# Performance work log

Hardware: AMD Instinct MI355X
Metric: run time of the kernel (lower is better)

The kernel has to match this reference:

```python
import jax, jax.numpy as jnp
import numpy as np

N_NODES = 50000
N_EDGES = 800000
IN_FEATS = 96
HIDDEN = 48


def setup_inputs() -> dict:
    key = jax.random.key(0)
    ks = jax.random.split(key, 16)
    x = jax.random.normal(ks[0], (N_NODES, IN_FEATS), dtype=jnp.float32)
    edge_index = jax.random.randint(ks[1], (2, N_EDGES), 0, N_NODES, dtype=jnp.int32)

    def lin(k, fan_in, fan_out):
        s = 1.0 / np.sqrt(fan_in)
        return jax.random.uniform(k, (fan_in, fan_out), jnp.float32, -s, s)

    return {
        "x": x,
        "edge_index": edge_index,
        # SAGEConv layer 0: in -> hidden
        "w_self0": lin(ks[2], IN_FEATS, HIDDEN),
        "w_neigh0": lin(ks[3], IN_FEATS, HIDDEN),
        "b0": jnp.zeros((HIDDEN,), jnp.float32),
        # SAGEConv layer 1: hidden -> hidden
        "w_self1": lin(ks[4], HIDDEN, HIDDEN),
        "w_neigh1": lin(ks[5], HIDDEN, HIDDEN),
        "b1": jnp.zeros((HIDDEN,), jnp.float32),
        # SAGEConv layer 2: hidden -> hidden
        "w_self2": lin(ks[6], HIDDEN, HIDDEN),
        "w_neigh2": lin(ks[7], HIDDEN, HIDDEN),
        "b2": jnp.zeros((HIDDEN,), jnp.float32),
        # prediction head: hidden -> 1
        "w_pred": lin(ks[8], HIDDEN, 1),
        "b_pred": jnp.zeros((1,), jnp.float32),
    }


def _sage_mean(x, src, dst, deg_inv, w_self, w_neigh, b):
    # mean over in-neighbors: gather src features, segment-sum at dst, / in-degree
    agg = jax.ops.segment_sum(x[src], dst, num_segments=N_NODES) * deg_inv  # [N, F]
    return x @ w_self + agg @ w_neigh + b


def reference(x, edge_index, w_self0, w_neigh0, b0, w_self1, w_neigh1, b1,
              w_self2, w_neigh2, b2, w_pred, b_pred):
    src, dst = edge_index[0], edge_index[1]
    deg = jax.ops.segment_sum(jnp.ones((src.shape[0],), x.dtype), dst,
                              num_segments=N_NODES)
    deg_inv = (1.0 / jnp.maximum(deg, 1.0))[:, None]  # isolated nodes -> 0 agg

    h = jax.nn.relu(_sage_mean(x, src, dst, deg_inv, w_self0, w_neigh0, b0))
    h = jax.nn.relu(_sage_mean(h, src, dst, deg_inv, w_self1, w_neigh1, b1))
    h = jax.nn.relu(_sage_mean(h, src, dst, deg_inv, w_self2, w_neigh2, b2))
    return h @ w_pred + b_pred  # [N, 1]
```

## Files before the change

kernel.cpp:

```cpp
#include <hip/hip_runtime.h>
#include <hip/hip_fp16.h>


constexpr int HID = 48;
constexpr int MAXDEG = 64;
constexpr int RSTRIDE = 64;
constexpr int GNB = 64;

__device__ __forceinline__ unsigned pack_h2(float a, float b) {
    __half2 h = __floats2half2_rn(a, b);
    return *reinterpret_cast<unsigned*>(&h);
}
__device__ __forceinline__ void acc_u2(float* g, uint2 u) {
    __half2 h0 = *reinterpret_cast<__half2*>(&u.x);
    __half2 h1 = *reinterpret_cast<__half2*>(&u.y);
    float2 f0 = __half22float2(h0), f1 = __half22float2(h1);
    g[0] += f0.x; g[1] += f0.y; g[2] += f1.x; g[3] += f1.y;
}
__device__ __forceinline__ void unpack_u2(float* v, uint2 u) {
    __half2 h0 = *reinterpret_cast<__half2*>(&u.x);
    __half2 h1 = *reinterpret_cast<__half2*>(&u.y);
    float2 f0 = __half22float2(h0), f1 = __half22float2(h1);
    v[0] = f0.x; v[1] = f0.y; v[2] = f1.x; v[3] = f1.y;
}
__device__ __forceinline__ void fma12_h(const uint2* __restrict__ wrow, float s,
                                        float* acc) {
    uint2 w0 = wrow[0], w1 = wrow[1], w2 = wrow[2];
    float v[12];
    unpack_u2(v + 0, w0); unpack_u2(v + 4, w1); unpack_u2(v + 8, w2);
#pragma unroll
    for (int j = 0; j < 12; ++j) acc[j] = fmaf(s, v[j], acc[j]);
}

template <int NB>
__device__ __forceinline__ void gather_pad(const __half* __restrict__ p,
                                           const unsigned short* __restrict__ bkt,
                                           const uint4 (&pw)[NB], int deg, int e,
                                           int jb, int zrow, float* g) {
    float ga[12], gb[12];
#pragma unroll
    for (int j = 0; j < 12; ++j) { ga[j] = 0.0f; gb[j] = 0.0f; }
    const int sh = 16 * e;
#pragma unroll
    for (int b = 0; b < NB; ++b) {
        const int k0 = 8 * b + e;
        int i0 = (k0 < deg)     ? (int)((pw[b].x >> sh) & 0xffffu) : zrow;
        int i1 = (k0 + 2 < deg) ? (int)((pw[b].y >> sh) & 0xffffu) : zrow;
        int i2 = (k0 + 4 < deg) ? (int)((pw[b].z >> sh) & 0xffffu) : zrow;
        int i3 = (k0 + 6 < deg) ? (int)((pw[b].w >> sh) & 0xffffu) : zrow;
        const uint2* r0 = reinterpret_cast<const uint2*>(p + (size_t)i0 * RSTRIDE + jb);
        const uint2* r1 = reinterpret_cast<const uint2*>(p + (size_t)i1 * RSTRIDE + jb);
        const uint2* r2 = reinterpret_cast<const uint2*>(p + (size_t)i2 * RSTRIDE + jb);
        const uint2* r3 = reinterpret_cast<const uint2*>(p + (size_t)i3 * RSTRIDE + jb);
        uint2 a0 = r0[0], a1 = r0[1], a2 = r0[2];
        uint2 b0 = r1[0], b1 = r1[1], b2 = r1[2];
        uint2 c0 = r2[0], c1 = r2[1], c2 = r2[2];
        uint2 d0 = r3[0], d1 = r3[1], d2 = r3[2];
        acc_u2(ga + 0, a0); acc_u2(ga + 4, a1); acc_u2(ga + 8, a2);
        acc_u2(gb + 0, b0); acc_u2(gb + 4, b1); acc_u2(gb + 8, b2);
        acc_u2(ga + 0, c0); acc_u2(ga + 4, c1); acc_u2(ga + 8, c2);
        acc_u2(gb + 0, d0); acc_u2(gb + 4, d1); acc_u2(gb + 8, d2);
    }
    int i = 8 * NB + e;
    for (; i + 6 < deg; i += 8) {
        int s0 = bkt[i], s1 = bkt[i + 2], s2 = bkt[i + 4], s3 = bkt[i + 6];
        const uint2* r0 = reinterpret_cast<const uint2*>(p + (size_t)s0 * RSTRIDE + jb);
        const uint2* r1 = reinterpret_cast<const uint2*>(p + (size_t)s1 * RSTRIDE + jb);
        const uint2* r2 = reinterpret_cast<const uint2*>(p + (size_t)s2 * RSTRIDE + jb);
        const uint2* r3 = reinterpret_cast<const uint2*>(p + (size_t)s3 * RSTRIDE + jb);
        uint2 a0 = r0[0], a1 = r0[1], a2 = r0[2];
        uint2 b0 = r1[0], b1 = r1[1], b2 = r1[2];
        uint2 c0 = r2[0], c1 = r2[1], c2 = r2[2];
        uint2 d0 = r3[0], d1 = r3[1], d2 = r3[2];
        acc_u2(ga + 0, a0); acc_u2(ga + 4, a1); acc_u2(ga + 8, a2);
        acc_u2(gb + 0, b0); acc_u2(gb + 4, b1); acc_u2(gb + 8, b2);
        acc_u2(ga + 0, c0); acc_u2(ga + 4, c1); acc_u2(ga + 8, c2);
        acc_u2(gb + 0, d0); acc_u2(gb + 4, d1); acc_u2(gb + 8, d2);
    }
    for (; i + 2 < deg; i += 4) {
        int s0 = bkt[i], s1 = bkt[i + 2];
        const uint2* r0 = reinterpret_cast<const uint2*>(p + (size_t)s0 * RSTRIDE + jb);
        const uint2* r1 = reinterpret_cast<const uint2*>(p + (size_t)s1 * RSTRIDE + jb);
        uint2 a0 = r0[0], a1 = r0[1], a2 = r0[2];
        uint2 b0 = r1[0], b1 = r1[1], b2 = r1[2];
        acc_u2(ga + 0, a0); acc_u2(ga + 4, a1); acc_u2(ga + 8, a2);
        acc_u2(gb + 0, b0); acc_u2(gb + 4, b1); acc_u2(gb + 8, b2);
    }
    if (i < deg) {
        const uint2* r0 = reinterpret_cast<const uint2*>(p + (size_t)bkt[i] * RSTRIDE + jb);
        uint2 a0 = r0[0], a1 = r0[1], a2 = r0[2];
        acc_u2(ga + 0, a0); acc_u2(ga + 4, a1); acc_u2(ga + 8, a2);
    }
#pragma unroll
    for (int j = 0; j < 12; ++j) g[j] = ga[j] + gb[j];
#pragma unroll
    for (int j = 0; j < 12; ++j) g[j] += __shfl_xor(g[j], 4, 64);
}

__global__ __launch_bounds__(128) void fill_proj_k(
    const float* __restrict__ X, const float* __restrict__ Wn,
    __half* __restrict__ p_out, int n_nodes,
    const int* __restrict__ src, const int* __restrict__ dst,
    int* __restrict__ cnt, unsigned short* __restrict__ buckets,
    int n_edges, int gemm_blocks, int cstride) {
    __shared__ float wlds[96 * HID];
    const int t = threadIdx.x;

    if ((int)blockIdx.x >= gemm_blocks) {
        int base = (blockIdx.x - gemm_blocks) * 512 + t;
#pragma unroll
        for (int u = 0; u < 4; ++u) {
            int eidx = base + u * 128;
            if (eidx < n_edges) {
                int d = dst[eidx];
                int s = src[eidx];
                int pos = atomicAdd(&cnt[(size_t)d * cstride], 1);
                if (pos < MAXDEG) buckets[(size_t)d * MAXDEG + pos] = (unsigned short)s;
            }
        }
        return;
    }

    if (blockIdx.x == 0 && t < 32)
        reinterpret_cast<unsigned*>(p_out + (size_t)n_nodes * RSTRIDE)[t] = 0u;

    const int q = t & 3;
    const int m = t >> 2;
    const int jb = q * 12;
    const int n0 = blockIdx.x * GNB + 2 * m;
    const int n1 = n0 + 1;
    const bool v0 = n0 < n_nodes, v1 = n1 < n_nodes;
    const int cn0 = v0 ? n0 : 0, cn1 = v1 ? n1 : 0;
    const float4* xr0 = reinterpret_cast<const float4*>(X + (size_t)cn0 * 96);
    const float4* xr1 = reinterpret_cast<const float4*>(X + (size_t)cn1 * 96);

    for (int i = t; i < 96 * HID; i += 128) wlds[i] = Wn[i];
    __syncthreads();

    float pa[12], pb[12];
#pragma unroll
    for (int j = 0; j < 12; ++j) { pa[j] = 0.0f; pb[j] = 0.0f; }
#pragma unroll 4
    for (int k4 = 0; k4 < 24; ++k4) {
        float4 xa = xr0[k4];
        float4 xb = xr1[k4];
#pragma unroll
        for (int c = 0; c < 4; ++c) {
            float x0 = (c == 0) ? xa.x : (c == 1) ? xa.y : (c == 2) ? xa.z : xa.w;
            float x1 = (c == 0) ? xb.x : (c == 1) ? xb.y : (c == 2) ? xb.z : xb.w;
            const float4* wr =
                reinterpret_cast<const float4*>(&wlds[(k4 * 4 + c) * HID + jb]);
#pragma unroll
            for (int j4 = 0; j4 < 3; ++j4) {
                float4 wv = wr[j4];
                pa[j4 * 4 + 0] = fmaf(x0, wv.x, pa[j4 * 4 + 0]);
                pa[j4 * 4 + 1] = fmaf(x0, wv.y, pa[j4 * 4 + 1]);
                pa[j4 * 4 + 2] = fmaf(x0, wv.z, pa[j4 * 4 + 2]);
                pa[j4 * 4 + 3] = fmaf(x0, wv.w, pa[j4 * 4 + 3]);
                pb[j4 * 4 + 0] = fmaf(x1, wv.x, pb[j4 * 4 + 0]);
                pb[j4 * 4 + 1] = fmaf(x1, wv.y, pb[j4 * 4 + 1]);
                pb[j4 * 4 + 2] = fmaf(x1, wv.z, pb[j4 * 4 + 2]);
                pb[j4 * 4 + 3] = fmaf(x1, wv.w, pb[j4 * 4 + 3]);
            }
        }
    }
    if (v0) {
        uint2* po = reinterpret_cast<uint2*>(p_out + (size_t)n0 * RSTRIDE + jb);
        po[0] = make_uint2(pack_h2(pa[0], pa[1]), pack_h2(pa[2], pa[3]));
        po[1] = make_uint2(pack_h2(pa[4], pa[5]), pack_h2(pa[6], pa[7]));
        po[2] = make_uint2(pack_h2(pa[8], pa[9]), pack_h2(pa[10], pa[11]));
    }
    if (v1) {
        uint2* po = reinterpret_cast<uint2*>(p_out + (size_t)n1 * RSTRIDE + jb);
        po[0] = make_uint2(pack_h2(pb[0], pb[1]), pack_h2(pb[2], pb[3]));
        po[1] = make_uint2(pack_h2(pb[4], pb[5]), pack_h2(pb[6], pb[7]));
        po[2] = make_uint2(pack_h2(pb[8], pb[9]), pack_h2(pb[10], pb[11]));
    }
}

__global__ __launch_bounds__(128, 4) void act_k(
    const __half* __restrict__ p_in, const float* __restrict__ X,
    const float* __restrict__ ws, const float* __restrict__ bias,
    const int* __restrict__ cnt, const unsigned short* __restrict__ buckets,
    __half* __restrict__ h_out, int n_nodes, int cstride) {
    __shared__ float wlds[96 * HID];
    __shared__ float b_lds[HID];

    const int t = threadIdx.x;
    if (blockIdx.x == 0 && t < 32)
        reinterpret_cast<unsigned*>(h_out + (size_t)n_nodes * RSTRIDE)[t] = 0u;

    const int q = t & 3;
    const int e = (t >> 2) & 1;
    const int m = t >> 3;
    const int n = blockIdx.x * 16 + m;
    const bool nv = n < n_nodes;
    const int cn = nv ? n : 0;
    const int jb = q * 12;

    const int deg_raw = cnt[(size_t)cn * cstride];
    const unsigned short* bkt = buckets + (size_t)cn * MAXDEG;
    uint4 pw[4];
#pragma unroll
    for (int b = 0; b < 4; ++b) pw[b] = reinterpret_cast<const uint4*>(bkt)[b];

    for (int i4 = t; i4 < 96 * HID / 4; i4 += 128)
        reinterpret_cast<float4*>(wlds)[i4] = reinterpret_cast<const float4*>(ws)[i4];
    if (t < HID) b_lds[t] = bias[t];
    __syncthreads();

    if (!nv) return;

    const int deg = min(deg_raw, MAXDEG);
    const float di = 1.0f / fmaxf((float)deg, 1.0f);

    float g[12];
    gather_pad<4>(p_in, bkt, pw, deg, e, jb, n_nodes, g);

    float s[12];
#pragma unroll
    for (int j = 0; j < 12; ++j) s[j] = (e == 0) ? b_lds[jb + j] : 0.0f;
    const float4* xr = reinterpret_cast<const float4*>(X + (size_t)cn * 96 + 48 * e);
#pragma unroll 4
    for (int k4 = 0; k4 < 12; ++k4) {
        float4 xv = xr[k4];
#pragma unroll
        for (int c = 0; c < 4; ++c) {
            float xc = (c == 0) ? xv.x : (c == 1) ? xv.y : (c == 2) ? xv.z : xv.w;
            const float4* wr = reinterpret_cast<const float4*>(
                &wlds[(48 * e + k4 * 4 + c) * HID + jb]);
#pragma unroll
            for (int j4 = 0; j4 < 3; ++j4) {
                float4 wv = wr[j4];
                s[j4 * 4 + 0] = fmaf(xc, wv.x, s[j4 * 4 + 0]);
                s[j4 * 4 + 1] = fmaf(xc, wv.y, s[j4 * 4 + 1]);
                s[j4 * 4 + 2] = fmaf(xc, wv.z, s[j4 * 4 + 2]);
                s[j4 * 4 + 3] = fmaf(xc, wv.w, s[j4 * 4 + 3]);
            }
        }
    }
#pragma unroll
    for (int j = 0; j < 12; ++j) s[j] += __shfl_xor(s[j], 4, 64);

    if (e == 0) {
        float h[12];
#pragma unroll
        for (int j = 0; j < 12; ++j) h[j] = fmaxf(fmaf(di, g[j], s[j]), 0.0f);
        uint2* ho = reinterpret_cast<uint2*>(h_out + (size_t)n * RSTRIDE + jb);
        ho[0] = make_uint2(pack_h2(h[0], h[1]), pack_h2(h[2], h[3]));
        ho[1] = make_uint2(pack_h2(h[4], h[5]), pack_h2(h[6], h[7]));
        ho[2] = make_uint2(pack_h2(h[8], h[9]), pack_h2(h[10], h[11]));
    }
}

template <bool LAST>
__global__ __launch_bounds__(128, 6) void layer_k(
    const __half* __restrict__ h_in, const int* __restrict__ cnt,
    const unsigned short* __restrict__ buckets, const float* __restrict__ wn,
    const float* __restrict__ ws, const float* __restrict__ bn,
    const float* __restrict__ w_pred, const float* __restrict__ b_pred,
    __half* __restrict__ h_out, float* __restrict__ out, int n_nodes,
    int cstride) {
    __shared__ uint2 wn_s[HID * HID / 4];
    __shared__ uint2 ws_s[HID * HID / 4];
    __shared__ float bn_lds[HID];
    __shared__ float wp_lds[HID];

    const int t = threadIdx.x;
    const int q = t & 3;
    const int e = (t >> 2) & 1;
    const int m = t >> 3;
    const int n = blockIdx.x * 16 + m;
    const bool nv = n < n_nodes;
    const int cn = nv ? n : 0;
    const int jb = q * 12;

    if (!LAST && blockIdx.x == 0 && t < 32)
        reinterpret_cast<unsigned*>(h_out + (size_t)n_nodes * RSTRIDE)[t] = 0u;

    const int deg_raw = cnt[(size_t)cn * cstride];
    const unsigned short* bkt = buckets + (size_t)cn * MAXDEG;
    uint4 pw[2];
#pragma unroll
    for (int b = 0; b < 2; ++b) pw[b] = reinterpret_cast<const uint4*>(bkt)[b];
    const uint2* hr = reinterpret_cast<const uint2*>(h_in + (size_t)cn * RSTRIDE + jb);
    uint2 ha = hr[0], hb = hr[1], hc = hr[2];

    for (int i4 = t; i4 < HID * HID / 4; i4 += 128) {
        float4 a = reinterpret_cast<const float4*>(wn)[i4];
        float4 b = reinterpret_cast<const float4*>(ws)[i4];
        wn_s[i4] = make_uint2(pack_h2(a.x, a.y), pack_h2(a.z, a.w));
        ws_s[i4] = make_uint2(pack_h2(b.x, b.y), pack_h2(b.z, b.w));
    }
    if (t < HID) bn_lds[t] = bn[t];
    if (LAST && t < HID) wp_lds[t] = w_pred[t];
    __syncthreads();

    if (!nv) return;

    const int deg = min(deg_raw, MAXDEG);
    const float di = 1.0f / fmaxf((float)deg, 1.0f);
    float g[12];
    gather_pad<2>(h_in, bkt, pw, deg, e, jb, n_nodes, g);
#pragma unroll
    for (int j = 0; j < 12; ++j) g[j] *= di;

    float hs_own[12];
    unpack_u2(hs_own + 0, ha); unpack_u2(hs_own + 4, hb); unpack_u2(hs_own + 8, hc);

    float acc[12];
#pragma unroll
    for (int j = 0; j < 12; ++j) acc[j] = (e == 0) ? bn_lds[jb + j] : 0.0f;

    const int kb = e * 24;
#pragma unroll
    for (int kk = 0; kk < 24; ++kk) {
        const int k = kb + kk;
        const int srcl = (t & ~3) | (k / 12);
        float gs = __shfl(g[kk % 12], srcl, 64);
        float hv = __shfl(hs_own[kk % 12], srcl, 64);
        fma12_h(&wn_s[(k * HID + jb) >> 2], gs, acc);
        fma12_h(&ws_s[(k * HID + jb) >> 2], hv, acc);
    }
#pragma unroll
    for (int j = 0; j < 12; ++j) acc[j] += __shfl_xor(acc[j], 4, 64);

    if (LAST) {
        float s = 0.0f;
#pragma unroll
        for (int j = 0; j < 12; ++j) s = fmaf(fmaxf(acc[j], 0.0f), wp_lds[jb + j], s);
        s += __shfl_xor(s, 1, 64);
        s += __shfl_xor(s, 2, 64);
        if ((t & 7) == 0) out[n] = s + b_pred[0];
        return;
    }

    if (e == 0) {
        float h[12];
#pragma unroll
        for (int j = 0; j < 12; ++j) h[j] = fmaxf(acc[j], 0.0f);
        uint2* ho = reinterpret_cast<uint2*>(h_out + (size_t)n * RSTRIDE + jb);
        ho[0] = make_uint2(pack_h2(h[0], h[1]), pack_h2(h[2], h[3]));
        ho[1] = make_uint2(pack_h2(h[4], h[5]), pack_h2(h[6], h[7]));
        ho[2] = make_uint2(pack_h2(h[8], h[9]), pack_h2(h[10], h[11]));
    }
}

extern "C" void kernel_launch(void* const* d_in, const int* in_sizes, int n_in,
                              void* d_out, int out_size, void* d_ws, size_t ws_size,
                              hipStream_t stream) {
    const float* x        = (const float*)d_in[0];
    const int*   ei       = (const int*)d_in[1];
    const float* w_self0  = (const float*)d_in[2];
    const float* w_neigh0 = (const float*)d_in[3];
    const float* b0       = (const float*)d_in[4];
    const float* w_self1  = (const float*)d_in[5];
    const float* w_neigh1 = (const float*)d_in[6];
    const float* b1       = (const float*)d_in[7];
    const float* w_self2  = (const float*)d_in[8];
    const float* w_neigh2 = (const float*)d_in[9];
    const float* b2       = (const float*)d_in[10];
    const float* w_pred   = (const float*)d_in[11];
    const float* b_pred   = (const float*)d_in[12];

    const int n_nodes = in_sizes[0] / 96;
    const int n_edges = in_sizes[1] / 2;
    const int* src = ei;
    const int* dst = ei + n_edges;

    const size_t need_fixed = (size_t)n_nodes * MAXDEG * 2
                            + 3 * ((size_t)(n_nodes + 1) * RSTRIDE * 2);
    int cstride = (need_fixed + (size_t)n_nodes * 4 * 4 <= ws_size) ? 4 : 1;

    char* wsb = (char*)d_ws;
    int* cnt                = (int*)wsb;              wsb += (size_t)n_nodes * cstride * 4;
    unsigned short* buckets = (unsigned short*)wsb;   wsb += (size_t)n_nodes * MAXDEG * 2;
    __half* p0 = (__half*)wsb;                        wsb += (size_t)(n_nodes + 1) * RSTRIDE * 2;
    __half* h1 = (__half*)wsb;                        wsb += (size_t)(n_nodes + 1) * RSTRIDE * 2;
    __half* h2 = (__half*)wsb;                        wsb += (size_t)(n_nodes + 1) * RSTRIDE * 2;
    float* out = (float*)d_out;

    const int gnb = (n_nodes + GNB - 1) / GNB;
    const int fb = (n_edges + 511) / 512;
    const int lb = (n_nodes + 15) / 16;

    hipMemsetAsync(cnt, 0, (size_t)n_nodes * cstride * 4, stream);

    fill_proj_k<<<gnb + fb, 128, 0, stream>>>(x, w_neigh0, p0, n_nodes, src, dst,
                                              cnt, buckets, n_edges, gnb, cstride);
    act_k<<<lb, 128, 0, stream>>>(p0, x, w_self0, b0, cnt, buckets, h1,
                                  n_nodes, cstride);
    layer_k<false><<<lb, 128, 0, stream>>>(h1, cnt, buckets, w_neigh1, w_self1,
                                           b1, nullptr, nullptr, h2, nullptr,
                                           n_nodes, cstride);
    layer_k<true><<<lb, 128, 0, stream>>>(h2, cnt, buckets, w_neigh2, w_self2,
                                          b2, w_pred, b_pred, nullptr, out,
                                          n_nodes, cstride);
}
```

Before: 215.4 us.

## Remap threads to 8-channel slices with 16-byte gathers instead of edge-split halves

Each node's 8 lanes now own 8 output channels each (6 active, 2 idle), and each lane gathers whole 16-byte chunks of every neighbor row. Previously lanes split the edges between two halves, used 8-byte loads and reduced across lanes with shuffles. The goal is wider memory transactions and no cross-lane reduction of the gathered sums. In exchange, 25% of lanes sit idle and each active lane walks every edge serially, so per-lane memory latency chains are longer. The dense projections are reorganized to match, and the layer-0 self projection no longer splits K across two lanes.

```diff
diff --git a/kernel.cpp b/kernel.cpp
--- a/kernel.cpp
+++ b/kernel.cpp
@@ -17,84 +17,66 @@
     float2 f0 = __half22float2(h0), f1 = __half22float2(h1);
     g[0] += f0.x; g[1] += f0.y; g[2] += f1.x; g[3] += f1.y;
 }
+__device__ __forceinline__ void acc_u4(float* g, uint4 u) {
+    acc_u2(g + 0, make_uint2(u.x, u.y));
+    acc_u2(g + 4, make_uint2(u.z, u.w));
+}
 __device__ __forceinline__ void unpack_u2(float* v, uint2 u) {
     __half2 h0 = *reinterpret_cast<__half2*>(&u.x);
     __half2 h1 = *reinterpret_cast<__half2*>(&u.y);
     float2 f0 = __half22float2(h0), f1 = __half22float2(h1);
     v[0] = f0.x; v[1] = f0.y; v[2] = f1.x; v[3] = f1.y;
 }
-__device__ __forceinline__ void fma12_h(const uint2* __restrict__ wrow, float s,
-                                        float* acc) {
-    uint2 w0 = wrow[0], w1 = wrow[1], w2 = wrow[2];
-    float v[12];
-    unpack_u2(v + 0, w0); unpack_u2(v + 4, w1); unpack_u2(v + 8, w2);
-#pragma unroll
-    for (int j = 0; j < 12; ++j) acc[j] = fmaf(s, v[j], acc[j]);
-}
-
-template <int NB>
-__device__ __forceinline__ void gather_pad(const __half* __restrict__ p,
-                                           const unsigned short* __restrict__ bkt,
-                                           const uint4 (&pw)[NB], int deg, int e,
-                                           int jb, int zrow, float* g) {
-    float ga[12], gb[12];
-#pragma unroll
-    for (int j = 0; j < 12; ++j) { ga[j] = 0.0f; gb[j] = 0.0f; }
-    const int sh = 16 * e;
-#pragma unroll
-    for (int b = 0; b < NB; ++b) {
-        const int k0 = 8 * b + e;
-        int i0 = (k0 < deg)     ? (int)((pw[b].x >> sh) & 0xffffu) : zrow;
-        int i1 = (k0 + 2 < deg) ? (int)((pw[b].y >> sh) & 0xffffu) : zrow;
-        int i2 = (k0 + 4 < deg) ? (int)((pw[b].z >> sh) & 0xffffu) : zrow;
-        int i3 = (k0 + 6 < deg) ? (int)((pw[b].w >> sh) & 0xffffu) : zrow;
-        const uint2* r0 = reinterpret_cast<const uint2*>(p + (size_t)i0 * RSTRIDE + jb);
-        const uint2* r1 = reinterpret_cast<const uint2*>(p + (size_t)i1 * RSTRIDE + jb);
-        const uint2* r2 = reinterpret_cast<const uint2*>(p + (size_t)i2 * RSTRIDE + jb);
-        const uint2* r3 = reinterpret_cast<const uint2*>(p + (size_t)i3 * RSTRIDE + jb);
-        uint2 a0 = r0[0], a1 = r0[1], a2 = r0[2];
-        uint2 b0 = r1[0], b1 = r1[1], b2 = r1[2];
-        uint2 c0 = r2[0], c1 = r2[1], c2 = r2[2];
-        uint2 d0 = r3[0], d1 = r3[1], d2 = r3[2];
-        acc_u2(ga + 0, a0); acc_u2(ga + 4, a1); acc_u2(ga + 8, a2);
-        acc_u2(gb + 0, b0); acc_u2(gb + 4, b1); acc_u2(gb + 8, b2);
-        acc_u2(ga + 0, c0); acc_u2(ga + 4, c1); acc_u2(ga + 8, c2);
-        acc_u2(gb + 0, d0); acc_u2(gb + 4, d1); acc_u2(gb + 8, d2);
-    }
-    int i = 8 * NB + e;
-    for (; i + 6 < deg; i += 8) {
-        int s0 = bkt[i], s1 = bkt[i + 2], s2 = bkt[i + 4], s3 = bkt[i + 6];
-        const uint2* r0 = reinterpret_cast<const uint2*>(p + (size_t)s0 * RSTRIDE + jb);
-        const uint2* r1 = reinterpret_cast<const uint2*>(p + (size_t)s1 * RSTRIDE + jb);
-        const uint2* r2 = reinterpret_cast<const uint2*>(p + (size_t)s2 * RSTRIDE + jb);
-        const uint2* r3 = reinterpret_cast<const uint2*>(p + (size_t)s3 * RSTRIDE + jb);
-        uint2 a0 = r0[0], a1 = r0[1], a2 = r0[2];
-        uint2 b0 = r1[0], b1 = r1[1], b2 = r1[2];
-        uint2 c0 = r2[0], c1 = r2[1], c2 = r2[2];
-        uint2 d0 = r3[0], d1 = r3[1], d2 = r3[2];
-        acc_u2(ga + 0, a0); acc_u2(ga + 4, a1); acc_u2(ga + 8, a2);
-        acc_u2(gb + 0, b0); acc_u2(gb + 4, b1); acc_u2(gb + 8, b2);
-        acc_u2(ga + 0, c0); acc_u2(ga + 4, c1); acc_u2(ga + 8, c2);
-        acc_u2(gb + 0, d0); acc_u2(gb + 4, d1); acc_u2(gb + 8, d2);
-    }
-    for (; i + 2 < deg; i += 4) {
-        int s0 = bkt[i], s1 = bkt[i + 2];
-        const uint2* r0 = reinterpret_cast<const uint2*>(p + (size_t)s0 * RSTRIDE + jb);
-        const uint2* r1 = reinterpret_cast<const uint2*>(p + (size_t)s1 * RSTRIDE + jb);
-        uint2 a0 = r0[0], a1 = r0[1], a2 = r0[2];
-        uint2 b0 = r1[0], b1 = r1[1], b2 = r1[2];
-        acc_u2(ga + 0, a0); acc_u2(ga + 4, a1); acc_u2(ga + 8, a2);
-        acc_u2(gb + 0, b0); acc_u2(gb + 4, b1); acc_u2(gb + 8, b2);
-    }
-    if (i < deg) {
-        const uint2* r0 = reinterpret_cast<const uint2*>(p + (size_t)bkt[i] * RSTRIDE + jb);
-        uint2 a0 = r0[0], a1 = r0[1], a2 = r0[2];
-        acc_u2(ga + 0, a0); acc_u2(ga + 4, a1); acc_u2(ga + 8, a2);
-    }
-#pragma unroll
-    for (int j = 0; j < 12; ++j) g[j] = ga[j] + gb[j];
-#pragma unroll
-    for (int j = 0; j < 12; ++j) g[j] += __shfl_xor(g[j], 4, 64);
+__device__ __forceinline__ void unpack_u4(float* v, uint4 u) {
+    unpack_u2(v + 0, make_uint2(u.x, u.y));
+    unpack_u2(v + 4, make_uint2(u.z, u.w));
+}
+
+__device__ __forceinline__ void gather_w(const __half* __restrict__ p,
+                                         const unsigned short* __restrict__ bkt,
+                                         const uint4 (&pw)[2], int deg,
+                                         int coff, int zrow, float* g) {
+    float ga[8], gb[8];
+#pragma unroll
+    for (int c = 0; c < 8; ++c) { ga[c] = 0.0f; gb[c] = 0.0f; }
+#pragma unroll
+    for (int b = 0; b < 2; ++b) {
+        const int k0 = 8 * b;
+        const unsigned w0 = pw[b].x, w1 = pw[b].y, w2 = pw[b].z, w3 = pw[b].w;
+        int i0 = (k0 + 0 < deg) ? (int)(w0 & 0xffffu) : zrow;
+        int i1 = (k0 + 1 < deg) ? (int)(w0 >> 16) : zrow;
+        int i2 = (k0 + 2 < deg) ? (int)(w1 & 0xffffu) : zrow;
+        int i3 = (k0 + 3 < deg) ? (int)(w1 >> 16) : zrow;
+        int i4 = (k0 + 4 < deg) ? (int)(w2 & 0xffffu) : zrow;
+        int i5 = (k0 + 5 < deg) ? (int)(w2 >> 16) : zrow;
+        int i6 = (k0 + 6 < deg) ? (int)(w3 & 0xffffu) : zrow;
+        int i7 = (k0 + 7 < deg) ? (int)(w3 >> 16) : zrow;
+        uint4 a0 = *reinterpret_cast<const uint4*>(p + (size_t)i0 * RSTRIDE + coff);
+        uint4 a1 = *reinterpret_cast<const uint4*>(p + (size_t)i1 * RSTRIDE + coff);
+        uint4 a2 = *reinterpret_cast<const uint4*>(p + (size_t)i2 * RSTRIDE + coff);
+        uint4 a3 = *reinterpret_cast<const uint4*>(p + (size_t)i3 * RSTRIDE + coff);
+        uint4 a4 = *reinterpret_cast<const uint4*>(p + (size_t)i4 * RSTRIDE + coff);
+        uint4 a5 = *reinterpret_cast<const uint4*>(p + (size_t)i5 * RSTRIDE + coff);
+        uint4 a6 = *reinterpret_cast<const uint4*>(p + (size_t)i6 * RSTRIDE + coff);
+        uint4 a7 = *reinterpret_cast<const uint4*>(p + (size_t)i7 * RSTRIDE + coff);
+        acc_u4(ga, a0); acc_u4(gb, a1); acc_u4(ga, a2); acc_u4(gb, a3);
+        acc_u4(ga, a4); acc_u4(gb, a5); acc_u4(ga, a6); acc_u4(gb, a7);
+    }
+    int i = 16;
+    for (; i + 3 < deg; i += 4) {
+        int s0 = bkt[i], s1 = bkt[i + 1], s2 = bkt[i + 2], s3 = bkt[i + 3];
+        uint4 a0 = *reinterpret_cast<const uint4*>(p + (size_t)s0 * RSTRIDE + coff);
+        uint4 a1 = *reinterpret_cast<const uint4*>(p + (size_t)s1 * RSTRIDE + coff);
+        uint4 a2 = *reinterpret_cast<const uint4*>(p + (size_t)s2 * RSTRIDE + coff);
+        uint4 a3 = *reinterpret_cast<const uint4*>(p + (size_t)s3 * RSTRIDE + coff);
+        acc_u4(ga, a0); acc_u4(gb, a1); acc_u4(ga, a2); acc_u4(gb, a3);
+    }
+    for (; i < deg; ++i) {
+        uint4 a0 = *reinterpret_cast<const uint4*>(p + (size_t)bkt[i] * RSTRIDE + coff);
+        acc_u4(ga, a0);
+    }
+#pragma unroll
+    for (int c = 0; c < 8; ++c) g[c] = ga[c] + gb[c];
 }
 
 __global__ __launch_bounds__(128) void fill_proj_k(
@@ -190,19 +172,19 @@
     if (blockIdx.x == 0 && t < 32)
         reinterpret_cast<unsigned*>(h_out + (size_t)n_nodes * RSTRIDE)[t] = 0u;
 
-    const int q = t & 3;
-    const int e = (t >> 2) & 1;
+    const int j = t & 7;
     const int m = t >> 3;
     const int n = blockIdx.x * 16 + m;
     const bool nv = n < n_nodes;
     const int cn = nv ? n : 0;
-    const int jb = q * 12;
+    const bool active = j < 6;
+    const int cb = active ? 8 * j : 0;
 
     const int deg_raw = cnt[(size_t)cn * cstride];
     const unsigned short* bkt = buckets + (size_t)cn * MAXDEG;
-    uint4 pw[4];
-#pragma unroll
-    for (int b = 0; b < 4; ++b) pw[b] = reinterpret_cast<const uint4*>(bkt)[b];
+    uint4 pw[2];
+#pragma unroll
+    for (int b = 0; b < 2; ++b) pw[b] = reinterpret_cast<const uint4*>(bkt)[b];
 
     for (int i4 = t; i4 < 96 * HID / 4; i4 += 128)
         reinterpret_cast<float4*>(wlds)[i4] = reinterpret_cast<const float4*>(ws)[i4];
@@ -214,43 +196,37 @@
     const int deg = min(deg_raw, MAXDEG);
     const float di = 1.0f / fmaxf((float)deg, 1.0f);
 
-    float g[12];
-    gather_pad<4>(p_in, bkt, pw, deg, e, jb, n_nodes, g);
-
-    float s[12];
-#pragma unroll
-    for (int j = 0; j < 12; ++j) s[j] = (e == 0) ? b_lds[jb + j] : 0.0f;
-    const float4* xr = reinterpret_cast<const float4*>(X + (size_t)cn * 96 + 48 * e);
+    float g[8];
+    if (active) gather_w(p_in, bkt, pw, deg, cb, n_nodes, g);
+
+    if (!active) return;
+
+    float s[8];
+#pragma unroll
+    for (int c = 0; c < 8; ++c) s[c] = b_lds[cb + c];
+    const float4* xr = reinterpret_cast<const float4*>(X + (size_t)cn * 96);
 #pragma unroll 4
-    for (int k4 = 0; k4 < 12; ++k4) {
+    for (int k4 = 0; k4 < 24; ++k4) {
         float4 xv = xr[k4];
 #pragma unroll
-        for (int c = 0; c < 4; ++c) {
-            float xc = (c == 0) ? xv.x : (c == 1) ? xv.y : (c == 2) ? xv.z : xv.w;
-            const float4* wr = reinterpret_cast<const float4*>(
-                &wlds[(48 * e + k4 * 4 + c) * HID + jb]);
-#pragma unroll
-            for (int j4 = 0; j4 < 3; ++j4) {
-                float4 wv = wr[j4];
-                s[j4 * 4 + 0] = fmaf(xc, wv.x, s[j4 * 4 + 0]);
-                s[j4 * 4 + 1] = fmaf(xc, wv.y, s[j4 * 4 + 1]);
-                s[j4 * 4 + 2] = fmaf(xc, wv.z, s[j4 * 4 + 2]);
-                s[j4 * 4 + 3] = fmaf(xc, wv.w, s[j4 * 4 + 3]);
-            }
-        }
-    }
-#pragma unroll
-    for (int j = 0; j < 12; ++j) s[j] += __shfl_xor(s[j], 4, 64);
-
-    if (e == 0) {
-        float h[12];
-#pragma unroll
-        for (int j = 0; j < 12; ++j) h[j] = fmaxf(fmaf(di, g[j], s[j]), 0.0f);
-        uint2* ho = reinterpret_cast<uint2*>(h_out + (size_t)n * RSTRIDE + jb);
-        ho[0] = make_uint2(pack_h2(h[0], h[1]), pack_h2(h[2], h[3]));
-        ho[1] = make_uint2(pack_h2(h[4], h[5]), pack_h2(h[6], h[7]));
-        ho[2] = make_uint2(pack_h2(h[8], h[9]), pack_h2(h[10], h[11]));
-    }
+        for (int c4 = 0; c4 < 4; ++c4) {
+            float xk = (c4 == 0) ? xv.x : (c4 == 1) ? xv.y : (c4 == 2) ? xv.z : xv.w;
+            const float4* wrk =
+                reinterpret_cast<const float4*>(&wlds[(k4 * 4 + c4) * HID + cb]);
+            float4 w0 = wrk[0], w1 = wrk[1];
+            s[0] = fmaf(xk, w0.x, s[0]); s[1] = fmaf(xk, w0.y, s[1]);
+            s[2] = fmaf(xk, w0.z, s[2]); s[3] = fmaf(xk, w0.w, s[3]);
+            s[4] = fmaf(xk, w1.x, s[4]); s[5] = fmaf(xk, w1.y, s[5]);
+            s[6] = fmaf(xk, w1.z, s[6]); s[7] = fmaf(xk, w1.w, s[7]);
+        }
+    }
+
+    float h[8];
+#pragma unroll
+    for (int c = 0; c < 8; ++c) h[c] = fmaxf(fmaf(di, g[c], s[c]), 0.0f);
+    uint4 o = make_uint4(pack_h2(h[0], h[1]), pack_h2(h[2], h[3]),
+                         pack_h2(h[4], h[5]), pack_h2(h[6], h[7]));
+    *reinterpret_cast<uint4*>(h_out + (size_t)n * RSTRIDE + cb) = o;
 }
 
 template <bool LAST>
@@ -261,19 +237,19 @@
     const float* __restrict__ w_pred, const float* __restrict__ b_pred,
     __half* __restrict__ h_out, float* __restrict__ out, int n_nodes,
     int cstride) {
-    __shared__ uint2 wn_s[HID * HID / 4];
-    __shared__ uint2 ws_s[HID * HID / 4];
+    __shared__ uint4 wn_s[HID * HID / 8];
+    __shared__ uint4 ws_s[HID * HID / 8];
     __shared__ float bn_lds[HID];
     __shared__ float wp_lds[HID];
 
     const int t = threadIdx.x;
-    const int q = t & 3;
-    const int e = (t >> 2) & 1;
+    const int j = t & 7;
     const int m = t >> 3;
     const int n = blockIdx.x * 16 + m;
     const bool nv = n < n_nodes;
     const int cn = nv ? n : 0;
-    const int jb = q * 12;
+    const bool active = j < 6;
+    const int cb = active ? 8 * j : 0;
 
     if (!LAST && blockIdx.x == 0 && t < 32)
         reinterpret_cast<unsigned*>(h_out + (size_t)n_nodes * RSTRIDE)[t] = 0u;
@@ -283,14 +259,17 @@
     uint4 pw[2];
 #pragma unroll
     for (int b = 0; b < 2; ++b) pw[b] = reinterpret_cast<const uint4*>(bkt)[b];
-    const uint2* hr = reinterpret_cast<const uint2*>(h_in + (size_t)cn * RSTRIDE + jb);
-    uint2 ha = hr[0], hb = hr[1], hc = hr[2];
-
-    for (int i4 = t; i4 < HID * HID / 4; i4 += 128) {
-        float4 a = reinterpret_cast<const float4*>(wn)[i4];
-        float4 b = reinterpret_cast<const float4*>(ws)[i4];
-        wn_s[i4] = make_uint2(pack_h2(a.x, a.y), pack_h2(a.z, a.w));
-        ws_s[i4] = make_uint2(pack_h2(b.x, b.y), pack_h2(b.z, b.w));
+    uint4 hv4 = *reinterpret_cast<const uint4*>(h_in + (size_t)cn * RSTRIDE + cb);
+
+    for (int i = t; i < HID * HID / 8; i += 128) {
+        const float4* wr = reinterpret_cast<const float4*>(wn) + i * 2;
+        float4 a = wr[0], b = wr[1];
+        wn_s[i] = make_uint4(pack_h2(a.x, a.y), pack_h2(a.z, a.w),
+                             pack_h2(b.x, b.y), pack_h2(b.z, b.w));
+        const float4* wr2 = reinterpret_cast<const float4*>(ws) + i * 2;
+        float4 a2 = wr2[0], b2 = wr2[1];
+        ws_s[i] = make_uint4(pack_h2(a2.x, a2.y), pack_h2(a2.z, a2.w),
+                             pack_h2(b2.x, b2.y), pack_h2(b2.z, b2.w));
     }
     if (t < HID) bn_lds[t] = bn[t];
     if (LAST && t < HID) wp_lds[t] = w_pred[t];
@@ -300,49 +279,62 @@
 
     const int deg = min(deg_raw, MAXDEG);
     const float di = 1.0f / fmaxf((float)deg, 1.0f);
-    float g[12];
-    gather_pad<2>(h_in, bkt, pw, deg, e, jb, n_nodes, g);
-#pragma unroll
-    for (int j = 0; j < 12; ++j) g[j] *= di;
-
-    float hs_own[12];
-    unpack_u2(hs_own + 0, ha); unpack_u2(hs_own + 4, hb); unpack_u2(hs_own + 8, hc);
-
-    float acc[12];
-#pragma unroll
-    for (int j = 0; j < 12; ++j) acc[j] = (e == 0) ? bn_lds[jb + j] : 0.0f;
-
-    const int kb = e * 24;
-#pragma unroll
-    for (int kk = 0; kk < 24; ++kk) {
-        const int k = kb + kk;
-        const int srcl = (t & ~3) | (k / 12);
-        float gs = __shfl(g[kk % 12], srcl, 64);
-        float hv = __shfl(hs_own[kk % 12], srcl, 64);
-        fma12_h(&wn_s[(k * HID + jb) >> 2], gs, acc);
-        fma12_h(&ws_s[(k * HID + jb) >> 2], hv, acc);
-    }
-#pragma unroll
-    for (int j = 0; j < 12; ++j) acc[j] += __shfl_xor(acc[j], 4, 64);
+    float g[8];
+    if (active) {
+        gather_w(h_in, bkt, pw, deg, cb, n_nodes, g);
+#pragma unroll
+        for (int c = 0; c < 8; ++c) g[c] *= di;
+    } else {
+#pragma unroll
+        for (int c = 0; c < 8; ++c) g[c] = 0.0f;
+    }
+
+    float hs[8];
+    unpack_u4(hs, hv4);
+
+    float acc[8];
+#pragma unroll
+    for (int c = 0; c < 8; ++c) acc[c] = active ? bn_lds[cb + c] : 0.0f;
+
+#pragma unroll
+    for (int jo = 0; jo < 6; ++jo) {
+        const int srcl = (t & ~7) | jo;
+#pragma unroll
+        for (int r = 0; r < 8; ++r) {
+            const int k = jo * 8 + r;
+            float gs = __shfl(g[r], srcl, 64);
+            float hv = __shfl(hs[r], srcl, 64);
+            uint4 wnv = wn_s[(k * HID + cb) >> 3];
+            uint4 wsv = ws_s[(k * HID + cb) >> 3];
+            float wa[8], wb[8];
+            unpack_u4(wa, wnv); unpack_u4(wb, wsv);
+#pragma unroll
+            for (int c = 0; c < 8; ++c)
+                acc[c] = fmaf(gs, wa[c], fmaf(hv, wb[c], acc[c]));
+        }
+    }
 
     if (LAST) {
-        float s = 0.0f;
-#pragma unroll
-        for (int j = 0; j < 12; ++j) s = fmaf(fmaxf(acc[j], 0.0f), wp_lds[jb + j], s);
-        s += __shfl_xor(s, 1, 64);
-        s += __shfl_xor(s, 2, 64);
-        if ((t & 7) == 0) out[n] = s + b_pred[0];
+        float sred = 0.0f;
+        if (active) {
+#pragma unroll
+            for (int c = 0; c < 8; ++c)
+                sred = fmaf(fmaxf(acc[c], 0.0f), wp_lds[cb + c], sred);
+        }
+        sred += __shfl_xor(sred, 1, 64);
+        sred += __shfl_xor(sred, 2, 64);
+        sred += __shfl_xor(sred, 4, 64);
+        if (j == 0) out[n] = sred + b_pred[0];
         return;
     }
 
-    if (e == 0) {
-        float h[12];
-#pragma unroll
-        for (int j = 0; j < 12; ++j) h[j] = fmaxf(acc[j], 0.0f);
-        uint2* ho = reinterpret_cast<uint2*>(h_out + (size_t)n * RSTRIDE + jb);
-        ho[0] = make_uint2(pack_h2(h[0], h[1]), pack_h2(h[2], h[3]));
-        ho[1] = make_uint2(pack_h2(h[4], h[5]), pack_h2(h[6], h[7]));
-        ho[2] = make_uint2(pack_h2(h[8], h[9]), pack_h2(h[10], h[11]));
+    if (active) {
+        float h[8];
+#pragma unroll
+        for (int c = 0; c < 8; ++c) h[c] = fmaxf(acc[c], 0.0f);
+        uint4 o = make_uint4(pack_h2(h[0], h[1]), pack_h2(h[2], h[3]),
+                             pack_h2(h[4], h[5]), pack_h2(h[6], h[7]));
+        *reinterpret_cast<uint4*>(h_out + (size_t)n * RSTRIDE + cb) = o;
     }
 }
 
```

Result: slower. 290.1 us (+34.7%).
